# Kernel optimization log

Hardware: AMD Instinct MI355X
Metric: run time of the kernel (lower is better)

The kernel has to match this reference:

```python
import jax, jax.numpy as jnp
import numpy as np


def setup_inputs() -> dict:
    key = jax.random.key(0)
    k1, k2, k3, k4 = jax.random.split(key, 4)
    B, V, NB, C, K, O = 2, 50000, 16, 64, 8, 64
    x = jax.random.normal(k1, (B, V, C), dtype=jnp.float32)
    # adj: 1-based neighbor indices, 0 == NULL (points at the zero pad row)
    adj = jax.random.randint(k2, (V, NB), 0, V + 1, dtype=jnp.int32)
    u = jax.random.normal(k3, (C, K), dtype=jnp.float32) * 0.05
    W = jax.random.normal(k4, (C, K * O), dtype=jnp.float32) * 0.05
    return {"x": x, "u": u, "W": W, "adj": adj}


def reference(x, u, W, adj):
    B, V, C = x.shape
    NB = adj.shape[1]
    K = u.shape[1]
    O = W.shape[1] // K

    # pad with zero row at index 0, gather neighbor patches: [B, V, NB, C]
    xp = jnp.concatenate([jnp.zeros((B, 1, C), x.dtype), x], axis=1)
    patches = xp[:, adj]

    # translation-invariant attention logits: (x_i - x_j) u, masked at NULL
    mask = (adj != 0)[None, :, :, None]            # [1, V, NB, 1]
    diff = jnp.where(mask, x[:, :, None, :] - patches, jnp.zeros((), x.dtype))
    q = jax.nn.softmax(jnp.einsum('bvnc,ck->bvnk', diff, u), axis=-1)  # softmax over kernel dim

    # per-vertex 1/deg (0 for isolated vertices)
    deg = jnp.sum(adj != 0, axis=-1).astype(x.dtype)   # [V]
    inv_deg = jnp.where(deg > 0, 1.0 / deg, jnp.zeros((), x.dtype))

    # fused (patches @ W) * q summed over neighbors and kernels -> [B, V, O]
    Wr = W.reshape(C, K, O)
    out = jnp.einsum('bvnc,cko,bvnk->bvo', patches, Wr, q)
    return out * inv_deg[None, :, None]
```

## Files before the change

### kernel.cpp

```cpp
#include <hip/hip_runtime.h>
#include <hip/hip_bf16.h>


constexpr int BB = 2;
constexpr int VV = 50000;
#define NB 16
#define CC 64
#define KK 8
#define OO 64
#define TV 16

typedef __attribute__((ext_vector_type(8))) short bf16x8;
typedef __attribute__((ext_vector_type(4))) float f32x4;

static __device__ __forceinline__ short f2b(float f) {
    __hip_bfloat16 h = __float2bfloat16(f);
    return *reinterpret_cast<short*>(&h);
}

constexpr int XUB = (BB * VV * 2 + 255) / 256;
constexpr int WPB = (CC * KK * OO) / 256;

__global__ void prep_kernel(const float* __restrict__ x,
                            const float* __restrict__ u,
                            float* __restrict__ xu,
                            const float* __restrict__ W,
                            short* __restrict__ Wb) {
    int blk = blockIdx.x;
    if (blk < XUB) {
        int t = blk * 256 + threadIdx.x;
        if (t >= BB * VV * 2) return;
        int g = t >> 1, half = t & 1;
        const float4* xr =
            reinterpret_cast<const float4*>(x) + (size_t)g * (CC / 4);
        const float4* u4 = reinterpret_cast<const float4*>(u);
        float a0 = 0.f, a1 = 0.f, a2 = 0.f, a3 = 0.f;
#pragma unroll
        for (int c4 = 0; c4 < CC / 4; ++c4) {
            float4 xv = xr[c4];
            float4 u0 = u4[(c4 * 4 + 0) * 2 + half];
            float4 u1 = u4[(c4 * 4 + 1) * 2 + half];
            float4 u2 = u4[(c4 * 4 + 2) * 2 + half];
            float4 u3 = u4[(c4 * 4 + 3) * 2 + half];
            a0 = fmaf(xv.x, u0.x, a0); a1 = fmaf(xv.x, u0.y, a1);
            a2 = fmaf(xv.x, u0.z, a2); a3 = fmaf(xv.x, u0.w, a3);
            a0 = fmaf(xv.y, u1.x, a0); a1 = fmaf(xv.y, u1.y, a1);
            a2 = fmaf(xv.y, u1.z, a2); a3 = fmaf(xv.y, u1.w, a3);
            a0 = fmaf(xv.z, u2.x, a0); a1 = fmaf(xv.z, u2.y, a1);
            a2 = fmaf(xv.z, u2.z, a2); a3 = fmaf(xv.z, u2.w, a3);
            a0 = fmaf(xv.w, u3.x, a0); a1 = fmaf(xv.w, u3.y, a1);
            a2 = fmaf(xv.w, u3.z, a2); a3 = fmaf(xv.w, u3.w, a3);
        }
        reinterpret_cast<float4*>(xu)[(size_t)g * 2 + half] =
            make_float4(a0, a1, a2, a3);
    } else {
        int dst = (blk - XUB) * 256 + threadIdx.x;
        int e = dst & 7;
        int l = (dst >> 3) & 63;
        int ctk = dst >> 9;
        int gct = ctk & 3;
        int ks = ctk >> 2;
        int ck = ks * 32 + (l >> 4) * 8 + e;
        int o = gct * 16 + (l & 15);
        Wb[dst] = f2b(W[ck * OO + o]);
    }
}

__global__ __launch_bounds__(256, 4) void feast_fused(
    const float* __restrict__ x, const int* __restrict__ adj,
    const float* __restrict__ xu, const short* __restrict__ Wb,
    float* __restrict__ out) {
    __shared__ char smem[TV * 1024];
    __shared__ float sInvd[TV];

    int t = threadIdx.x;
    int b = blockIdx.y;
    int v0 = blockIdx.x * TV;
    int vl = t >> 4;
    int jj = t & 15;
    int v = v0 + vl;

    float* qlds = reinterpret_cast<float*>(smem);
    const float4* xu4 = reinterpret_cast<const float4*>(xu);
    const float4* x4 = reinterpret_cast<const float4*>(x);

    int off[NB];
    float deg = 0.f;
    {
        const int4* arow = reinterpret_cast<const int4*>(adj + (size_t)v * NB);
#pragma unroll
        for (int n4 = 0; n4 < 4; ++n4) {
            int4 t4 = arow[n4];
            int aa[4] = {t4.x, t4.y, t4.z, t4.w};
#pragma unroll
            for (int s = 0; s < 4; ++s) {
                int an = aa[s];
                deg += (an != 0) ? 1.f : 0.f;
                off[n4 * 4 + s] = (b * VV + (an ? an - 1 : 0)) * 16 + jj;
            }
        }
    }
    if (jj == 0) sInvd[vl] = (deg > 0.f) ? (1.f / deg) : 0.f;

    {
        int gs = b * VV + v;
        float4 s0 = xu4[(size_t)gs * 2], s1 = xu4[(size_t)gs * 2 + 1];
        int an = adj[(size_t)v * NB + jj];
        int g = b * VV + (an ? an - 1 : 0);
        float4 n0 = xu4[(size_t)g * 2], n1 = xu4[(size_t)g * 2 + 1];
        float l8[KK] = {s0.x - n0.x, s0.y - n0.y, s0.z - n0.z, s0.w - n0.w,
                        s1.x - n1.x, s1.y - n1.y, s1.z - n1.z, s1.w - n1.w};
        float mx = l8[0];
#pragma unroll
        for (int k = 1; k < KK; ++k) mx = fmaxf(mx, l8[k]);
        float e8[KK];
        float sum = 0.f;
#pragma unroll
        for (int k = 0; k < KK; ++k) {
            e8[k] = __expf(l8[k] - mx);
            sum += e8[k];
        }
        float r = an ? (1.f / sum) : 0.f;
        f32x4* qp = reinterpret_cast<f32x4*>(qlds + jj * 128 + vl * 8);
        qp[0] = (f32x4){e8[0] * r, e8[1] * r, e8[2] * r, e8[3] * r};
        qp[1] = (f32x4){e8[4] * r, e8[5] * r, e8[6] * r, e8[7] * r};
    }

#define CONS(n, P)                                                             \
    {                                                                          \
        const f32x4* qv =                                                      \
            reinterpret_cast<const f32x4*>(qlds + (n) * 128 + vl * 8);         \
        f32x4 q0 = qv[0];                                                      \
        f32x4 q1 = qv[1];                                                      \
        float p[4] = {P.x, P.y, P.z, P.w};                                     \
        _Pragma("unroll") for (int c = 0; c < 4; ++c) {                        \
            _Pragma("unroll") for (int k = 0; k < 4; ++k) {                    \
                acc[c][k] = fmaf(p[c], q0[k], acc[c][k]);                      \
                acc[c][k + 4] = fmaf(p[c], q1[k], acc[c][k + 4]);              \
            }                                                                  \
        }                                                                      \
    }

    float4 P0, P1, P2, P3, P4, P5;
    P0 = x4[off[0]];
    P1 = x4[off[1]];
    P2 = x4[off[2]];
    P3 = x4[off[3]];
    P4 = x4[off[4]];
    P5 = x4[off[5]];
    __syncthreads();

    float acc[4][KK];
#pragma unroll
    for (int c = 0; c < 4; ++c)
#pragma unroll
        for (int k = 0; k < KK; ++k) acc[c][k] = 0.f;

    CONS(0, P0) P0 = x4[off[6]];
    CONS(1, P1) P1 = x4[off[7]];
    CONS(2, P2) P2 = x4[off[8]];
    CONS(3, P3) P3 = x4[off[9]];
    CONS(4, P4) P4 = x4[off[10]];
    CONS(5, P5) P5 = x4[off[11]];
    CONS(6, P0) P0 = x4[off[12]];
    CONS(7, P1) P1 = x4[off[13]];
    CONS(8, P2) P2 = x4[off[14]];
    CONS(9, P3) P3 = x4[off[15]];
    CONS(10, P4)
    CONS(11, P5)
    CONS(12, P0)
    CONS(13, P1)
    CONS(14, P2)
    CONS(15, P3)

    __syncthreads();

#pragma unroll
    for (int s = 0; s < 4; ++s) {
        bf16x8 w;
#pragma unroll
        for (int k = 0; k < KK; ++k) w[k] = f2b(acc[s][k]);
        int slot = jj * 4 + s;
        int slot2 = slot ^ ((slot >> 3) & 7) ^ (vl & 7);
        *reinterpret_cast<bf16x8*>(smem + vl * 1024 + slot2 * 16) = w;
    }
    __syncthreads();

    {
        int wid = t >> 6;
        int l = t & 63;
        int r = l & 15;

        f32x4 acc2 = (f32x4){0.f, 0.f, 0.f, 0.f};
        const bf16x8* WbV = reinterpret_cast<const bf16x8*>(Wb);

#pragma unroll
        for (int ks = 0; ks < 16; ++ks) {
            int ks4h = ks * 4 + (l >> 4);
            int slotA = ks4h ^ ((ks4h >> 3) & 7) ^ (r & 7);
            bf16x8 afrag = *reinterpret_cast<const bf16x8*>(
                smem + r * 1024 + slotA * 16);
            bf16x8 bfrag = WbV[(ks * 4 + wid) * 64 + l];
            acc2 = __builtin_amdgcn_mfma_f32_16x16x32_bf16(afrag, bfrag, acc2,
                                                           0, 0, 0);
        }

        int col = wid * 16 + (l & 15);
#pragma unroll
        for (int jr = 0; jr < 4; ++jr) {
            int rowl = (l >> 4) * 4 + jr;
            out[((size_t)b * VV + v0 + rowl) * OO + col] =
                acc2[jr] * sInvd[rowl];
        }
    }
}

extern "C" void kernel_launch(void* const* d_in, const int* in_sizes, int n_in,
                              void* d_out, int out_size, void* d_ws,
                              size_t ws_size, hipStream_t stream) {
    const float* x = (const float*)d_in[0];
    const float* u = (const float*)d_in[1];
    const float* W = (const float*)d_in[2];
    const int* adj = (const int*)d_in[3];
    float* out = (float*)d_out;

    float* xu = (float*)d_ws;
    short* Wb = (short*)((char*)d_ws + (size_t)BB * VV * KK * sizeof(float));

    prep_kernel<<<XUB + WPB, 256, 0, stream>>>(x, u, xu, W, Wb);
    dim3 g(VV / TV, BB);
    feast_fused<<<g, 256, 0, stream>>>(x, adj, xu, Wb, out);
}
```

Measured before the change: 164.6 us.

## Halve vertices per block and split channels across 32 lanes per vertex

Each block now handles 8 vertices instead of 16. Each vertex gets 32 threads that each own 2 channels (float2 gathers) instead of 16 threads with 4 channels. This shrinks the per-thread accumulator and raises the launch-bounds occupancy target. It also deepens prefetch to 8 neighbor loads in flight. The MFMA stage still computes 16 rows, half of them over uninitialized LDS, and their output stores are masked off. The aim is more latency hiding for the random gathers, paid for with narrower loads, wasted MFMA rows and idle threads during the softmax stage.

```diff
diff --git a/kernel.cpp b/kernel.cpp
--- a/kernel.cpp
+++ b/kernel.cpp
@@ -8,7 +8,7 @@
 #define CC 64
 #define KK 8
 #define OO 64
-#define TV 16
+#define TV 8
 
 typedef __attribute__((ext_vector_type(8))) short bf16x8;
 typedef __attribute__((ext_vector_type(4))) float f32x4;
@@ -66,23 +66,23 @@
     }
 }
 
-__global__ __launch_bounds__(256, 4) void feast_fused(
+__global__ __launch_bounds__(256, 8) void feast_fused(
     const float* __restrict__ x, const int* __restrict__ adj,
     const float* __restrict__ xu, const short* __restrict__ Wb,
     float* __restrict__ out) {
-    __shared__ char smem[TV * 1024];
+    __shared__ char smem[16 * 1024];
     __shared__ float sInvd[TV];
 
     int t = threadIdx.x;
     int b = blockIdx.y;
     int v0 = blockIdx.x * TV;
-    int vl = t >> 4;
-    int jj = t & 15;
+    int vl = t >> 5;
+    int jj = t & 31;
     int v = v0 + vl;
 
     float* qlds = reinterpret_cast<float*>(smem);
     const float4* xu4 = reinterpret_cast<const float4*>(xu);
-    const float4* x4 = reinterpret_cast<const float4*>(x);
+    const float2* x2 = reinterpret_cast<const float2*>(x);
 
     int off[NB];
     float deg = 0.f;
@@ -96,16 +96,19 @@
             for (int s = 0; s < 4; ++s) {
                 int an = aa[s];
                 deg += (an != 0) ? 1.f : 0.f;
-                off[n4 * 4 + s] = (b * VV + (an ? an - 1 : 0)) * 16 + jj;
+                off[n4 * 4 + s] = (b * VV + (an ? an - 1 : 0)) * 32 + jj;
             }
         }
     }
     if (jj == 0) sInvd[vl] = (deg > 0.f) ? (1.f / deg) : 0.f;
 
-    {
-        int gs = b * VV + v;
+    if (t < 128) {
+        int pav = t >> 4;
+        int pan = t & 15;
+        int pv = v0 + pav;
+        int gs = b * VV + pv;
         float4 s0 = xu4[(size_t)gs * 2], s1 = xu4[(size_t)gs * 2 + 1];
-        int an = adj[(size_t)v * NB + jj];
+        int an = adj[(size_t)pv * NB + pan];
         int g = b * VV + (an ? an - 1 : 0);
         float4 n0 = xu4[(size_t)g * 2], n1 = xu4[(size_t)g * 2 + 1];
         float l8[KK] = {s0.x - n0.x, s0.y - n0.y, s0.z - n0.z, s0.w - n0.w,
@@ -121,7 +124,7 @@
             sum += e8[k];
         }
         float r = an ? (1.f / sum) : 0.f;
-        f32x4* qp = reinterpret_cast<f32x4*>(qlds + jj * 128 + vl * 8);
+        f32x4* qp = reinterpret_cast<f32x4*>(qlds + pan * 64 + pav * 8);
         qp[0] = (f32x4){e8[0] * r, e8[1] * r, e8[2] * r, e8[3] * r};
         qp[1] = (f32x4){e8[4] * r, e8[5] * r, e8[6] * r, e8[7] * r};
     }
@@ -129,58 +132,59 @@
 #define CONS(n, P)                                                             \
     {                                                                          \
         const f32x4* qv =                                                      \
-            reinterpret_cast<const f32x4*>(qlds + (n) * 128 + vl * 8);         \
+            reinterpret_cast<const f32x4*>(qlds + (n) * 64 + vl * 8);          \
         f32x4 q0 = qv[0];                                                      \
         f32x4 q1 = qv[1];                                                      \
-        float p[4] = {P.x, P.y, P.z, P.w};                                     \
-        _Pragma("unroll") for (int c = 0; c < 4; ++c) {                        \
-            _Pragma("unroll") for (int k = 0; k < 4; ++k) {                    \
-                acc[c][k] = fmaf(p[c], q0[k], acc[c][k]);                      \
-                acc[c][k + 4] = fmaf(p[c], q1[k], acc[c][k + 4]);              \
-            }                                                                  \
+        _Pragma("unroll") for (int k = 0; k < 4; ++k) {                        \
+            acc[0][k] = fmaf(P.x, q0[k], acc[0][k]);                           \
+            acc[0][k + 4] = fmaf(P.x, q1[k], acc[0][k + 4]);                   \
+            acc[1][k] = fmaf(P.y, q0[k], acc[1][k]);                           \
+            acc[1][k + 4] = fmaf(P.y, q1[k], acc[1][k + 4]);                   \
         }                                                                      \
     }
 
-    float4 P0, P1, P2, P3, P4, P5;
-    P0 = x4[off[0]];
-    P1 = x4[off[1]];
-    P2 = x4[off[2]];
-    P3 = x4[off[3]];
-    P4 = x4[off[4]];
-    P5 = x4[off[5]];
+    float2 P0, P1, P2, P3, P4, P5, P6, P7;
+    P0 = x2[off[0]];
+    P1 = x2[off[1]];
+    P2 = x2[off[2]];
+    P3 = x2[off[3]];
+    P4 = x2[off[4]];
+    P5 = x2[off[5]];
+    P6 = x2[off[6]];
+    P7 = x2[off[7]];
     __syncthreads();
 
-    float acc[4][KK];
-#pragma unroll
-    for (int c = 0; c < 4; ++c)
+    float acc[2][KK];
+#pragma unroll
+    for (int c = 0; c < 2; ++c)
 #pragma unroll
         for (int k = 0; k < KK; ++k) acc[c][k] = 0.f;
 
-    CONS(0, P0) P0 = x4[off[6]];
-    CONS(1, P1) P1 = x4[off[7]];
-    CONS(2, P2) P2 = x4[off[8]];
-    CONS(3, P3) P3 = x4[off[9]];
-    CONS(4, P4) P4 = x4[off[10]];
-    CONS(5, P5) P5 = x4[off[11]];
-    CONS(6, P0) P0 = x4[off[12]];
-    CONS(7, P1) P1 = x4[off[13]];
-    CONS(8, P2) P2 = x4[off[14]];
-    CONS(9, P3) P3 = x4[off[15]];
-    CONS(10, P4)
-    CONS(11, P5)
-    CONS(12, P0)
-    CONS(13, P1)
-    CONS(14, P2)
-    CONS(15, P3)
+    CONS(0, P0) P0 = x2[off[8]];
+    CONS(1, P1) P1 = x2[off[9]];
+    CONS(2, P2) P2 = x2[off[10]];
+    CONS(3, P3) P3 = x2[off[11]];
+    CONS(4, P4) P4 = x2[off[12]];
+    CONS(5, P5) P5 = x2[off[13]];
+    CONS(6, P6) P6 = x2[off[14]];
+    CONS(7, P7) P7 = x2[off[15]];
+    CONS(8, P0)
+    CONS(9, P1)
+    CONS(10, P2)
+    CONS(11, P3)
+    CONS(12, P4)
+    CONS(13, P5)
+    CONS(14, P6)
+    CONS(15, P7)
 
     __syncthreads();
 
 #pragma unroll
-    for (int s = 0; s < 4; ++s) {
+    for (int s = 0; s < 2; ++s) {
         bf16x8 w;
 #pragma unroll
         for (int k = 0; k < KK; ++k) w[k] = f2b(acc[s][k]);
-        int slot = jj * 4 + s;
+        int slot = 2 * jj + s;
         int slot2 = slot ^ ((slot >> 3) & 7) ^ (vl & 7);
         *reinterpret_cast<bf16x8*>(smem + vl * 1024 + slot2 * 16) = w;
     }
@@ -209,8 +213,10 @@
 #pragma unroll
         for (int jr = 0; jr < 4; ++jr) {
             int rowl = (l >> 4) * 4 + jr;
-            out[((size_t)b * VV + v0 + rowl) * OO + col] =
-                acc2[jr] * sInvd[rowl];
+            if (rowl < TV) {
+                out[((size_t)b * VV + v0 + rowl) * OO + col] =
+                    acc2[jr] * sInvd[rowl];
+            }
         }
     }
 }
```

Measured after the change: 259.6 us. +57.7%, slower.
